# Kernel optimization log

Measured on AMD Instinct MI355X. Metric: run time of the kernel, lower is better.

## Reference

```python
import jax, jax.numpy as jnp
import numpy as np

RES = 64
C_DIM = 64
N_BLOCKS = 4
EPS = 1e-12


def conv2d(x, w, b, pad):
    out = jax.lax.conv_general_dilated(
        x, w, window_strides=(1, 1), padding=[(pad, pad), (pad, pad)],
        dimension_numbers=('NCHW', 'OIHW', 'NCHW'))
    return out + b[None, :, None, None]


def unfold3(x):
    # F.unfold(kernel=3, padding=1): [B,C,H,W] -> [B, C*9, H*W], torch ordering (c, ki, kj)
    B, C, H, W = x.shape
    xp = jnp.pad(x, ((0, 0), (0, 0), (1, 1), (1, 1)))
    patches = jnp.stack([xp[:, :, ki:ki + H, kj:kj + W]
                         for ki in range(3) for kj in range(3)], axis=2)  # [B,C,9,H,W]
    return patches.reshape(B, C * 9, H * W)


def fold3(t, H, W):
    # F.fold(kernel=3, padding=1): sum overlapping patches back to [B,C,H,W]
    B, C9, L = t.shape
    C = C9 // 9
    t = t.reshape(B, C, 3, 3, H, W)
    out = jnp.zeros((B, C, H + 2, W + 2), t.dtype)
    for ki in range(3):
        for kj in range(3):
            out = out.at[:, :, ki:ki + H, kj:kj + W].add(t[:, :, ki, kj])
    return out[:, :, 1:H + 1, 1:W + 1]


def setup_inputs() -> dict:
    key = jax.random.key(0)
    ks = jax.random.split(key, 16)
    B, L, C = 4, RES * RES, C_DIM
    s = 0.05
    inp = {
        'c0': jax.random.normal(ks[0], (B, L, C), jnp.float32),
        'f0': jax.random.normal(ks[1], (B, L, C), jnp.float32),
        'c1': jax.random.normal(ks[2], (B, L, C), jnp.float32),
        'head_w': jax.random.normal(ks[3], (C, C, 5, 5), jnp.float32) * s,
        'head_b': jax.random.normal(ks[4], (C,), jnp.float32) * s,
        'rb_w1': jax.random.normal(ks[5], (N_BLOCKS, C, C, 3, 3), jnp.float32) * s,
        'rb_b1': jax.random.normal(ks[6], (N_BLOCKS, C), jnp.float32) * s,
        'rb_w2': jax.random.normal(ks[7], (N_BLOCKS, C, C, 3, 3), jnp.float32) * s,
        'rb_b2': jax.random.normal(ks[8], (N_BLOCKS, C), jnp.float32) * s,
        'tail_w': jax.random.normal(ks[9], (C, C, 5, 5), jnp.float32) * s,
        'tail_b': jax.random.normal(ks[10], (C,), jnp.float32) * s,
        'sq_w': jax.random.normal(ks[11], (C, 2 * C, 5, 5), jnp.float32) * s,
        'sq_b': jax.random.normal(ks[12], (C,), jnp.float32) * s,
    }
    return inp


def reference(c0, f0, c1, head_w, head_b, rb_w1, rb_b1, rb_w2, rb_b2,
              tail_w, tail_b, sq_w, sq_b):
    B, L, C = c1.shape
    H = W = RES
    c1 = c1.swapaxes(1, 2).reshape(B, C, H, W)
    c0 = c0.swapaxes(1, 2).reshape(B, C, H, W)
    f0 = f0.swapaxes(1, 2).reshape(B, C, H, W)
    Delta_c = c1 - c0

    # --- search_Trans: patch correlation + best-match texture transfer ---
    c1u = unfold3(c1)                       # [B, C9, L]
    c0u = unfold3(c0).swapaxes(1, 2)        # [B, L, C9]
    c0n = c0u / jnp.maximum(jnp.linalg.norm(c0u, axis=2, keepdims=True), EPS)
    c1n = c1u / jnp.maximum(jnp.linalg.norm(c1u, axis=1, keepdims=True), EPS)
    R = jnp.einsum('blk,bkm->blm', c0n, c1n)  # [B, L, L]
    R_star = jnp.max(R, axis=1)               # [B, L]
    R_arg = jnp.argmax(R, axis=1)              # [B, L]
    f0u = unfold3(f0)                          # [B, C9, L]
    Tu = jnp.take_along_axis(f0u, R_arg[:, None, :], axis=2)
    T = fold3(Tu, H, W) / 9.0                  # [B, C, H, W]
    S = R_star.reshape(B, 1, H, W)

    # --- residual conv stack on Delta_c ---
    x1 = conv2d(Delta_c, head_w, head_b, 2)
    x = x1
    for i in range(rb_w1.shape[0]):  # NOTE: original feeds x1 into every block
        h = jax.nn.relu(conv2d(x1, rb_w1[i], rb_b1[i], 1))
        x = conv2d(h, rb_w2[i], rb_b2[i], 1) + x1
    x = conv2d(x, tail_w, tail_b, 2)
    Delta_c_fea = x + x1

    x = conv2d(jnp.concatenate([Delta_c_fea, T], axis=1), sq_w, sq_b, 2)
    out = Delta_c_fea + x * S
    return out.reshape(B, C, L).swapaxes(1, 2)
```

## Files before the change

### kernel.cpp

```cpp
#include <hip/hip_runtime.h>
#include <hip/hip_bf16.h>


#define BATCH 4

typedef unsigned short u16;
typedef unsigned int   u32;
typedef __attribute__((ext_vector_type(8))) short short8;
typedef __attribute__((ext_vector_type(4))) float f32x4;

__device__ __forceinline__ void bsplit2(float a, float b, u32& ho, u32& lo) {
  __hip_bfloat16 ha = __float2bfloat16(a), hb = __float2bfloat16(b);
  float ra = a - __bfloat162float(ha), rb = b - __bfloat162float(hb);
  __hip_bfloat16 la = __float2bfloat16(ra), lb = __float2bfloat16(rb);
  ho = (u32)*(u16*)&ha | ((u32)*(u16*)&hb << 16);
  lo = (u32)*(u16*)&la | ((u32)*(u16*)&lb << 16);
}

__device__ __forceinline__ void gload_lds16(const void* g, void* l) {
  __builtin_amdgcn_global_load_lds((const __attribute__((address_space(1))) void*)g,
                                   (__attribute__((address_space(3))) void*)l, 16, 0, 0);
}

__global__ __launch_bounds__(256) void prep_ss(const float* __restrict__ c0,
    const float* __restrict__ c1, float* __restrict__ ss0, float* __restrict__ ss1)
{
  int tid = blockIdx.x * 256 + threadIdx.x;
  const float* p0 = c0 + (size_t)tid * 64;
  const float* p1 = c1 + (size_t)tid * 64;
  float s0 = 0.f, s1 = 0.f;
  for (int c = 0; c < 64; ++c) {
    float a = p0[c]; s0 += a * a;
    float b = p1[c]; s1 += b * b;
  }
  ss0[tid] = s0;
  ss1[tid] = s1;
}

__global__ __launch_bounds__(256) void norm_kernel(const float* __restrict__ ss0,
    const float* __restrict__ ss1, float* __restrict__ inv0, float* __restrict__ inv1)
{
  int tid = blockIdx.x * 256 + threadIdx.x;
  int b = tid >> 12, l = tid & 4095;
  int y = l >> 6, x = l & 63;
  int base = b << 12;
  float s0 = 0.f, s1 = 0.f;
  for (int dy = -1; dy <= 1; ++dy) {
    int yy = y + dy; if (yy < 0 || yy >= 64) continue;
    for (int dx = -1; dx <= 1; ++dx) {
      int xx = x + dx; if (xx < 0 || xx >= 64) continue;
      int ii = base + (yy << 6) + xx;
      s0 += ss0[ii]; s1 += ss1[ii];
    }
  }
  inv0[tid] = 1.f / fmaxf(sqrtf(s0), 1e-12f);
  inv1[tid] = 1.f / fmaxf(sqrtf(s1), 1e-12f);
}

__global__ __launch_bounds__(256) void split_pad_kernel(const float* __restrict__ c0,
    const float* __restrict__ c1, u16* __restrict__ p0h, u16* __restrict__ p0l,
    u16* __restrict__ p1h, u16* __restrict__ p1l)
{
  int b = blockIdx.y, t = threadIdx.x;
  int pix = blockIdx.x * 4 + (t >> 6);
  int c = t & 63;
  int py = pix / 66, px = pix - py * 66;
  size_t d = ((size_t)b * 4356 + pix) * 64 + c;
  float v0 = 0.f, v1 = 0.f;
  if (py >= 1 && py <= 64 && px >= 1 && px <= 64) {
    size_t s = (((size_t)b << 12) + ((py - 1) << 6) + (px - 1)) * 64 + c;
    v0 = c0[s]; v1 = c1[s];
  }
  __hip_bfloat16 h = __float2bfloat16(v0);
  float r = v0 - __bfloat162float(h);
  __hip_bfloat16 lo = __float2bfloat16(r);
  p0h[d] = *(u16*)&h; p0l[d] = *(u16*)&lo;
  h = __float2bfloat16(v1);
  r = v1 - __bfloat162float(h);
  lo = __float2bfloat16(r);
  p1h[d] = *(u16*)&h; p1l[d] = *(u16*)&lo;
}

__global__ __launch_bounds__(256) void wprep(const float* __restrict__ src,
    u16* __restrict__ wh, u16* __restrict__ wl, int Cin, int KK, int n)
{
  int i = blockIdx.x * 256 + threadIdx.x;
  if (i >= n) return;
  int per = Cin * KK;
  int cout = i / per;
  int rem = i - cout * per;
  int cin = rem / KK;
  int tap = rem - cin * KK;
  float x = src[i];
  __hip_bfloat16 h = __float2bfloat16(x);
  float r = x - __bfloat162float(h);
  __hip_bfloat16 lo = __float2bfloat16(r);
  int d = (tap * 64 + cout) * Cin + cin;
  wh[d] = *(u16*)&h;
  wl[d] = *(u16*)&lo;
}

__global__ __launch_bounds__(256) void corr_mfma(const u16* __restrict__ p0h,
    const u16* __restrict__ p0l, const u16* __restrict__ p1h, const u16* __restrict__ p1l,
    const float* __restrict__ inv0, float* __restrict__ pval, int* __restrict__ pidx)
{
  __shared__ __align__(16) u16 smem[32768];
  int mt = blockIdx.x, lt = blockIdx.y, b = blockIdx.z;
  int t = threadIdx.x;
  int lane = t & 63, w = t >> 6;
  int wl = w >> 1, wm = w & 1;
  int cc = lane & 15, q = lane >> 4;
  const size_t boff = (size_t)b * 278784;
  const u16* msrc = (w == 0) ? p0h : (w == 1) ? p0l : (w == 2) ? p1h : p1l;
  msrc += boff;
  const float* inv0b = inv0 + (b << 12);
  int isB = w >> 1;

  int srow0 = lane >> 2;
  int cs_g  = (lane & 3) ^ ((lane >> 3) & 3);
  int sw    = (cc >> 1) & 3;

  auto stage = [&](int ssub, int sph, u16* dst) {
    int r = sph >> 1, hh = sph & 1;
    int ki = r / 3, kj = r - ki * 3;
    int pb = isB ? (mt << 7) : ((lt << 9) + (ssub << 7));
#pragma unroll
    for (int it = 0; it < 8; ++it) {
      int p = pb + (it << 4) + srow0;
      int ypad = (p >> 6) + ki, xpad = (p & 63) + kj;
      const u16* g = msrc + (((size_t)(ypad * 66 + xpad)) << 6) + (hh << 5) + (cs_g << 3);
      gload_lds16(g, dst + (it << 9));
    }
  };

  float bval[4] = {-1e30f, -1e30f, -1e30f, -1e30f};
  int   bidx[4] = {0, 0, 0, 0};

  stage(0, 0, smem + (w << 12));

  for (int sub = 0; sub < 4; ++sub) {
    int row0 = (lt << 9) + (sub << 7);
    f32x4 acc[4][4];
#pragma unroll
    for (int i = 0; i < 4; ++i)
#pragma unroll
      for (int j = 0; j < 4; ++j) acc[i][j] = (f32x4){0.f, 0.f, 0.f, 0.f};

    for (int ph = 0; ph < 18; ++ph) {
      int g = sub * 18 + ph;
      int nxt = g + 1;
      if (nxt < 72) {
        int np = ph + 1, ns = sub;
        if (np == 18) { np = 0; ++ns; }
        stage(ns, np, smem + ((nxt & 1) << 14) + (w << 12));
        asm volatile("s_waitcnt vmcnt(8)" ::: "memory");
      } else {
        asm volatile("s_waitcnt vmcnt(0)" ::: "memory");
      }
      __builtin_amdgcn_s_barrier();
      __builtin_amdgcn_sched_barrier(0);
      const u16* bb = smem + ((g & 1) << 14);
      short8 afh[4], afl[4], bfh[4], bfl[4];
#pragma unroll
      for (int i = 0; i < 4; ++i) {
        int ra = (((wl << 6) + (i << 4) + cc) << 5) + ((q ^ sw) << 3);
        afh[i] = *(const short8*)(&bb[ra]);
        afl[i] = *(const short8*)(&bb[4096 + ra]);
      }
#pragma unroll
      for (int j = 0; j < 4; ++j) {
        int rb = (((wm << 6) + (j << 4) + cc) << 5) + ((q ^ sw) << 3);
        bfh[j] = *(const short8*)(&bb[8192 + rb]);
        bfl[j] = *(const short8*)(&bb[12288 + rb]);
      }
#pragma unroll
      for (int i = 0; i < 4; ++i)
#pragma unroll
        for (int j = 0; j < 4; ++j) {
          acc[i][j] = __builtin_amdgcn_mfma_f32_16x16x32_bf16(afh[i], bfl[j], acc[i][j], 0, 0, 0);
          acc[i][j] = __builtin_amdgcn_mfma_f32_16x16x32_bf16(afl[i], bfh[j], acc[i][j], 0, 0, 0);
          acc[i][j] = __builtin_amdgcn_mfma_f32_16x16x32_bf16(afh[i], bfh[j], acc[i][j], 0, 0, 0);
        }
      __builtin_amdgcn_sched_barrier(0);
      __builtin_amdgcn_s_barrier();
    }
#pragma unroll
    for (int i = 0; i < 4; ++i) {
#pragma unroll
      for (int rg = 0; rg < 4; ++rg) {
        int l = row0 + (wl << 6) + (i << 4) + (q << 2) + rg;
        float sc = inv0b[l];
#pragma unroll
        for (int j = 0; j < 4; ++j) {
          float v = acc[i][j][rg] * sc;
          if (v > bval[j]) { bval[j] = v; bidx[j] = l; }
        }
      }
    }
  }

  __syncthreads();
  float* lval = (float*)smem;
  int*   lidx = (int*)((char*)smem + 4096);
  int slot = (wl << 2) + q;
#pragma unroll
  for (int j = 0; j < 4; ++j) {
    int col = (wm << 6) + (j << 4) + cc;
    lval[col * 8 + slot] = bval[j];
    lidx[col * 8 + slot] = bidx[j];
  }
  __syncthreads();
  if (t < 128) {
    float bv = -1e30f; int bi = 0x7FFFFFFF;
    for (int s = 0; s < 8; ++s) {
      float v = lval[t * 8 + s]; int id = lidx[t * 8 + s];
      if (v > bv || (v == bv && id < bi)) { bv = v; bi = id; }
    }
    size_t o = (size_t)(((b << 3) + lt) << 12) + (mt << 7) + t;
    pval[o] = bv; pidx[o] = bi;
  }
}

__global__ __launch_bounds__(256) void reduce_kernel(const float* __restrict__ pval,
    const int* __restrict__ pidx, const float* __restrict__ inv1,
    float* __restrict__ S, int* __restrict__ arg)
{
  int tid = blockIdx.x * 256 + threadIdx.x;
  int b = tid >> 12, m = tid & 4095;
  float bv = -1e30f; int bi = 0x7FFFFFFF;
  for (int lt = 0; lt < 8; ++lt) {
    size_t o = (size_t)(((b << 3) + lt) << 12) + m;
    float v = pval[o]; int id = pidx[o];
    if (v > bv || (v == bv && id < bi)) { bv = v; bi = id; }
  }
  S[tid] = bv * inv1[tid];
  arg[tid] = ((unsigned)bi < 4096u) ? bi : 0;
}

__global__ __launch_bounds__(256) void tgather_kernel(const float* __restrict__ f0,
    const int* __restrict__ arg, float* __restrict__ T)
{
  __shared__ int a3[192];
  int y = blockIdx.x, b = blockIdx.y, t = threadIdx.x;
  if (t < 192) {
    int r = t >> 6, xx = t & 63;
    int yy = y + r - 1;
    a3[t] = (yy >= 0 && yy < 64) ? arg[(b << 12) + (yy << 6) + xx] : 0;
  }
  __syncthreads();
  int c = t & 63, pg = t >> 6;
  for (int it = 0; it < 16; ++it) {
    int px = pg + (it << 2);
    float sum = 0.f;
#pragma unroll
    for (int ki = 0; ki < 3; ++ki) {
      int yn = y + 1 - ki;
      if (yn < 0 || yn >= 64) continue;
#pragma unroll
      for (int kj = 0; kj < 3; ++kj) {
        int xn = px + 1 - kj;
        if (xn < 0 || xn >= 64) continue;
        int p = a3[((2 - ki) << 6) + xn];
        int sy = (p >> 6) + ki - 1, sx = (p & 63) + kj - 1;
        if (sy >= 0 && sy < 64 && sx >= 0 && sx < 64)
          sum += f0[((((size_t)b << 12) + (sy << 6) + sx) << 6) + c];
      }
    }
    T[((((size_t)b << 12) + (y << 6) + px)) * 64 + c] = sum * (1.f / 9.f);
  }
}

template<int KS, int CINCH>
__global__ __launch_bounds__(256) void conv_mfma(const float* __restrict__ in0,
    const float* __restrict__ in1, const u16* __restrict__ whp, const u16* __restrict__ wlp,
    const float* __restrict__ bias, float* __restrict__ outp,
    const float* __restrict__ res, int dorelu, int dm)
{
  constexpr int P = KS / 2;
  constexpr int CIN = CINCH * 32;
  constexpr int KSH = (CINCH == 2) ? 1 : 2;
  constexpr int NIT = KS * KS * CINCH;
  __shared__ __align__(16) u16 Ah[2][32 * 40], Al[2][32 * 40];
  __shared__ __align__(16) u16 Bh[2][64 * 40], Bl[2][64 * 40];
  int tile = blockIdx.x, b = blockIdx.y;
  int t = threadIdx.x;
  int lane = t & 63, w = t >> 6;
  int wpx = w >> 1, wm = w & 1;
  int cc = lane & 15, q = lane >> 4;
  int ty = tile >> 1, txb = (tile & 1) << 5;
  const size_t abase = (size_t)b << 12;
  f32x4 acc[2];
  acc[0] = (f32x4){0.f, 0.f, 0.f, 0.f};
  acc[1] = (f32x4){0.f, 0.f, 0.f, 0.f};

  uint4 rg[4];
  int arow = t >> 2, acs = t & 3;
  int tb = t - 128;

  auto issue_loads = [&](int itn) {
    int tapn = itn >> KSH, kkn = itn & (CINCH - 1);
    int ki = tapn / KS, kj = tapn - ki * KS;
    if (t < 128) {
      rg[0] = rg[1] = rg[2] = rg[3] = make_uint4(0u, 0u, 0u, 0u);
      int iy = ty + ki - P;
      int ix = txb + arow + kj - P;
      if ((unsigned)iy < 64u && (unsigned)ix < 64u) {
        size_t base = (abase + (iy << 6) + ix) << 6;
        int cg = kkn * 32 + (acs << 3);
        if (dm) {
          rg[0] = *(const uint4*)(in0 + base + cg);
          rg[1] = *(const uint4*)(in0 + base + cg + 4);
          rg[2] = *(const uint4*)(in1 + base + cg);
          rg[3] = *(const uint4*)(in1 + base + cg + 4);
        } else {
          const float* sp = (CINCH == 4 && cg >= 64) ? (in1 + base + (cg - 64))
                                                     : (in0 + base + cg);
          rg[0] = *(const uint4*)sp;
          rg[1] = *(const uint4*)(sp + 4);
        }
      }
    } else {
#pragma unroll
      for (int rr = 0; rr < 2; ++rr) {
        int idx = tb * 2 + rr;
        int cout = idx >> 2, cs = idx & 3;
        size_t so = (size_t)(tapn * 64 + cout) * CIN + kkn * 32 + (cs << 3);
        rg[rr]     = *(const uint4*)&whp[so];
        rg[2 + rr] = *(const uint4*)&wlp[so];
      }
    }
  };

  auto write_lds = [&](int cur) {
    if (t < 128) {
      float v[8];
      if (dm) {
#pragma unroll
        for (int e = 0; e < 4; ++e) {
          v[e]     = __uint_as_float((&rg[2].x)[e]) - __uint_as_float((&rg[0].x)[e]);
          v[4 + e] = __uint_as_float((&rg[3].x)[e]) - __uint_as_float((&rg[1].x)[e]);
        }
      } else {
#pragma unroll
        for (int e = 0; e < 4; ++e) {
          v[e]     = __uint_as_float((&rg[0].x)[e]);
          v[4 + e] = __uint_as_float((&rg[1].x)[e]);
        }
      }
      uint4 uh, ul;
      bsplit2(v[0], v[1], uh.x, ul.x);
      bsplit2(v[2], v[3], uh.y, ul.y);
      bsplit2(v[4], v[5], uh.z, ul.z);
      bsplit2(v[6], v[7], uh.w, ul.w);
      *(uint4*)&Ah[cur][arow * 40 + (acs << 3)] = uh;
      *(uint4*)&Al[cur][arow * 40 + (acs << 3)] = ul;
    } else {
#pragma unroll
      for (int rr = 0; rr < 2; ++rr) {
        int idx = tb * 2 + rr;
        int cout = idx >> 2, cs = idx & 3;
        *(uint4*)&Bh[cur][cout * 40 + (cs << 3)] = rg[rr];
        *(uint4*)&Bl[cur][cout * 40 + (cs << 3)] = rg[2 + rr];
      }
    }
  };

  issue_loads(0);
  for (int it = 0; it < NIT; ++it) {
    int cur = it & 1;
    write_lds(cur);
    if (it + 1 < NIT) issue_loads(it + 1);
    asm volatile("s_waitcnt lgkmcnt(0)" ::: "memory");
    __builtin_amdgcn_s_barrier();
    __builtin_amdgcn_sched_barrier(0);
    short8 afh, afl, bfh[2], bfl[2];
    {
      int ra = ((wpx << 4) + cc) * 40 + (q << 3);
      afh = *(const short8*)&Ah[cur][ra];
      afl = *(const short8*)&Al[cur][ra];
    }
#pragma unroll
    for (int j = 0; j < 2; ++j) {
      int rb = ((wm << 5) + (j << 4) + cc) * 40 + (q << 3);
      bfh[j] = *(const short8*)&Bh[cur][rb];
      bfl[j] = *(const short8*)&Bl[cur][rb];
    }
#pragma unroll
    for (int j = 0; j < 2; ++j) {
      acc[j] = __builtin_amdgcn_mfma_f32_16x16x32_bf16(afh, bfl[j], acc[j], 0, 0, 0);
      acc[j] = __builtin_amdgcn_mfma_f32_16x16x32_bf16(afl, bfh[j], acc[j], 0, 0, 0);
      acc[j] = __builtin_amdgcn_mfma_f32_16x16x32_bf16(afh, bfh[j], acc[j], 0, 0, 0);
    }
  }
#pragma unroll
  for (int rgi = 0; rgi < 4; ++rgi) {
    int p = (ty << 6) + txb + (wpx << 4) + (q << 2) + rgi;
#pragma unroll
    for (int j = 0; j < 2; ++j) {
      int cout = (wm << 5) + (j << 4) + cc;
      float v = acc[j][rgi] + bias[cout];
      if (dorelu) v = fmaxf(v, 0.f);
      size_t oi = ((abase + p) << 6) + cout;
      if (res) v += res[oi];
      outp[oi] = v;
    }
  }
}

__global__ __launch_bounds__(256) void final_kernel(const float* __restrict__ dcf,
    const float* __restrict__ xs, const float* __restrict__ S, float* __restrict__ out)
{
  int tid = blockIdx.x * 256 + threadIdx.x;
  out[tid] = dcf[tid] + xs[tid] * S[tid >> 6];
}

extern "C" void kernel_launch(void* const* d_in, const int* in_sizes, int n_in,
                              void* d_out, int out_size, void* d_ws, size_t ws_size,
                              hipStream_t stream)
{
  (void)in_sizes; (void)n_in; (void)out_size; (void)ws_size;
  const float* c0     = (const float*)d_in[0];
  const float* f0     = (const float*)d_in[1];
  const float* c1     = (const float*)d_in[2];
  const float* head_w = (const float*)d_in[3];
  const float* head_b = (const float*)d_in[4];
  const float* rb_w1  = (const float*)d_in[5];
  const float* rb_b1  = (const float*)d_in[6];
  const float* rb_w2  = (const float*)d_in[7];
  const float* rb_b2  = (const float*)d_in[8];
  const float* tail_w = (const float*)d_in[9];
  const float* tail_b = (const float*)d_in[10];
  const float* sq_w   = (const float*)d_in[11];
  const float* sq_b   = (const float*)d_in[12];
  float* out = (float*)d_out;
  char* ws = (char*)d_ws;

  const size_t OFF_SS0  = 0;
  const size_t OFF_SS1  = 65536;
  const size_t OFF_INV0 = 131072;
  const size_t OFF_INV1 = 196608;
  const size_t OFF_S    = 262144;
  const size_t OFF_ARG  = 327680;
  const size_t OFF_PVAL = 393216;
  const size_t OFF_PIDX = 917504;
  const size_t OFF_WHH  = 1441792;
  const size_t OFF_WHL  = 1646592;
  const size_t OFF_W1H  = 1851392;
  const size_t OFF_W1L  = 1925120;
  const size_t OFF_W2H  = 1998848;
  const size_t OFF_W2L  = 2072576;
  const size_t OFF_WTH  = 2146304;
  const size_t OFF_WTL  = 2351104;
  const size_t OFF_WSH  = 2555904;
  const size_t OFF_WSL  = 2965504;
  const size_t OFF_P0H  = 3375104;
  const size_t OFF_P0L  = OFF_P0H + 2230272;
  const size_t OFF_P1H  = OFF_P0L + 2230272;
  const size_t OFF_P1L  = OFF_P1H + 2230272;
  const size_t OFF_SA   = 3375104;
  const size_t OFF_SB   = 7569408;
  const size_t OFF_SC   = 11763712;

  float* ss0  = (float*)(ws + OFF_SS0);
  float* ss1  = (float*)(ws + OFF_SS1);
  float* inv0 = (float*)(ws + OFF_INV0);
  float* inv1 = (float*)(ws + OFF_INV1);
  float* Sbuf = (float*)(ws + OFF_S);
  int*   argb = (int*)(ws + OFF_ARG);
  float* pval = (float*)(ws + OFF_PVAL);
  int*   pidx = (int*)(ws + OFF_PIDX);
  u16* whh = (u16*)(ws + OFF_WHH); u16* whl = (u16*)(ws + OFF_WHL);
  u16* w1h = (u16*)(ws + OFF_W1H); u16* w1l = (u16*)(ws + OFF_W1L);
  u16* w2h = (u16*)(ws + OFF_W2H); u16* w2l = (u16*)(ws + OFF_W2L);
  u16* wth = (u16*)(ws + OFF_WTH); u16* wtl = (u16*)(ws + OFF_WTL);
  u16* wsh = (u16*)(ws + OFF_WSH); u16* wsl = (u16*)(ws + OFF_WSL);
  u16* p0h = (u16*)(ws + OFF_P0H); u16* p0l = (u16*)(ws + OFF_P0L);
  u16* p1h = (u16*)(ws + OFF_P1H); u16* p1l = (u16*)(ws + OFF_P1L);
  float* x1  = (float*)(ws + OFF_SA);
  float* Tb  = (float*)(ws + OFF_SA);
  float* hb  = (float*)(ws + OFF_SB);
  float* dcf = (float*)(ws + OFF_SB);
  float* xb  = (float*)(ws + OFF_SC);
  float* xsb = (float*)(ws + OFF_SC);

  dim3 b256(256);
  prep_ss<<<dim3(64), b256, 0, stream>>>(c0, c1, ss0, ss1);
  norm_kernel<<<dim3(64), b256, 0, stream>>>(ss0, ss1, inv0, inv1);
  split_pad_kernel<<<dim3(1089, BATCH), b256, 0, stream>>>(c0, c1, p0h, p0l, p1h, p1l);
  wprep<<<dim3(400), b256, 0, stream>>>(head_w, whh, whl, 64, 25, 102400);
  wprep<<<dim3(144), b256, 0, stream>>>(rb_w1 + 110592, w1h, w1l, 64, 9, 36864);
  wprep<<<dim3(144), b256, 0, stream>>>(rb_w2 + 110592, w2h, w2l, 64, 9, 36864);
  wprep<<<dim3(400), b256, 0, stream>>>(tail_w, wth, wtl, 64, 25, 102400);
  wprep<<<dim3(800), b256, 0, stream>>>(sq_w, wsh, wsl, 128, 25, 204800);

  corr_mfma<<<dim3(32, 8, BATCH), b256, 0, stream>>>(p0h, p0l, p1h, p1l, inv0, pval, pidx);
  reduce_kernel<<<dim3(64), b256, 0, stream>>>(pval, pidx, inv1, Sbuf, argb);

  dim3 cgrid(128, BATCH);
  conv_mfma<5, 2><<<cgrid, b256, 0, stream>>>(c0, c1, whh, whl, head_b, x1, nullptr, 0, 1);
  conv_mfma<3, 2><<<cgrid, b256, 0, stream>>>(x1, nullptr, w1h, w1l, rb_b1 + 192, hb, nullptr, 1, 0);
  conv_mfma<3, 2><<<cgrid, b256, 0, stream>>>(hb, nullptr, w2h, w2l, rb_b2 + 192, xb, x1, 0, 0);
  conv_mfma<5, 2><<<cgrid, b256, 0, stream>>>(xb, nullptr, wth, wtl, tail_b, dcf, x1, 0, 0);

  tgather_kernel<<<dim3(64, BATCH), b256, 0, stream>>>(f0, argb, Tb);
  conv_mfma<5, 4><<<cgrid, b256, 0, stream>>>(dcf, Tb, wsh, wsl, sq_b, xsb, nullptr, 0, 0);

  final_kernel<<<dim3(4096), b256, 0, stream>>>(dcf, xsb, Sbuf, out);
}
```

Baseline: 529.4 us.

## Fuse sum-of-squares into split_pad, widen conv K-step, fuse final epilogue

The per-pixel sum-of-squares is now computed inside split_pad_kernel with a wave shuffle reduction, which removes the separate prep_ss pass over c0/c1. The conv_mfma main loop now consumes 64 input channels per iteration instead of 32, with an LDS stride of 72. This halves the number of barriers and loop iterations at the cost of more registers. The final out = dcf + x*S step moves into the squeeze conv's epilogue, removing final_kernel and one intermediate buffer round trip. Register pressure from rg[8] and v[16] may reduce occupancy.

```diff
diff --git a/kernel.cpp b/kernel.cpp
--- a/kernel.cpp
+++ b/kernel.cpp
@@ -20,21 +20,6 @@
 __device__ __forceinline__ void gload_lds16(const void* g, void* l) {
   __builtin_amdgcn_global_load_lds((const __attribute__((address_space(1))) void*)g,
                                    (__attribute__((address_space(3))) void*)l, 16, 0, 0);
-}
-
-__global__ __launch_bounds__(256) void prep_ss(const float* __restrict__ c0,
-    const float* __restrict__ c1, float* __restrict__ ss0, float* __restrict__ ss1)
-{
-  int tid = blockIdx.x * 256 + threadIdx.x;
-  const float* p0 = c0 + (size_t)tid * 64;
-  const float* p1 = c1 + (size_t)tid * 64;
-  float s0 = 0.f, s1 = 0.f;
-  for (int c = 0; c < 64; ++c) {
-    float a = p0[c]; s0 += a * a;
-    float b = p1[c]; s1 += b * b;
-  }
-  ss0[tid] = s0;
-  ss1[tid] = s1;
 }
 
 __global__ __launch_bounds__(256) void norm_kernel(const float* __restrict__ ss0,
@@ -59,15 +44,17 @@
 
 __global__ __launch_bounds__(256) void split_pad_kernel(const float* __restrict__ c0,
     const float* __restrict__ c1, u16* __restrict__ p0h, u16* __restrict__ p0l,
-    u16* __restrict__ p1h, u16* __restrict__ p1l)
+    u16* __restrict__ p1h, u16* __restrict__ p1l,
+    float* __restrict__ ss0, float* __restrict__ ss1)
 {
   int b = blockIdx.y, t = threadIdx.x;
   int pix = blockIdx.x * 4 + (t >> 6);
   int c = t & 63;
   int py = pix / 66, px = pix - py * 66;
   size_t d = ((size_t)b * 4356 + pix) * 64 + c;
+  bool interior = (py >= 1 && py <= 64 && px >= 1 && px <= 64);
   float v0 = 0.f, v1 = 0.f;
-  if (py >= 1 && py <= 64 && px >= 1 && px <= 64) {
+  if (interior) {
     size_t s = (((size_t)b << 12) + ((py - 1) << 6) + (px - 1)) * 64 + c;
     v0 = c0[s]; v1 = c1[s];
   }
@@ -79,6 +66,17 @@
   r = v1 - __bfloat162float(h);
   lo = __float2bfloat16(r);
   p1h[d] = *(u16*)&h; p1l[d] = *(u16*)&lo;
+  float s0 = v0 * v0, s1 = v1 * v1;
+#pragma unroll
+  for (int off = 32; off; off >>= 1) {
+    s0 += __shfl_xor(s0, off);
+    s1 += __shfl_xor(s1, off);
+  }
+  if (c == 0 && interior) {
+    int sstid = (b << 12) + ((py - 1) << 6) + (px - 1);
+    ss0[sstid] = s0;
+    ss1[sstid] = s1;
+  }
 }
 
 __global__ __launch_bounds__(256) void wprep(const float* __restrict__ src,
@@ -274,14 +272,15 @@
 __global__ __launch_bounds__(256) void conv_mfma(const float* __restrict__ in0,
     const float* __restrict__ in1, const u16* __restrict__ whp, const u16* __restrict__ wlp,
     const float* __restrict__ bias, float* __restrict__ outp,
-    const float* __restrict__ res, int dorelu, int dm)
+    const float* __restrict__ res, const float* __restrict__ smul, int dorelu, int dm)
 {
   constexpr int P = KS / 2;
   constexpr int CIN = CINCH * 32;
-  constexpr int KSH = (CINCH == 2) ? 1 : 2;
-  constexpr int NIT = KS * KS * CINCH;
-  __shared__ __align__(16) u16 Ah[2][32 * 40], Al[2][32 * 40];
-  __shared__ __align__(16) u16 Bh[2][64 * 40], Bl[2][64 * 40];
+  constexpr int NKH = CINCH / 2;
+  constexpr int NIT = KS * KS * NKH;
+  constexpr int AST = 72;
+  __shared__ __align__(16) u16 Ah[2][32 * AST], Al[2][32 * AST];
+  __shared__ __align__(16) u16 Bh[2][64 * AST], Bl[2][64 * AST];
   int tile = blockIdx.x, b = blockIdx.y;
   int t = threadIdx.x;
   int lane = t & 63, w = t >> 6;
@@ -293,74 +292,82 @@
   acc[0] = (f32x4){0.f, 0.f, 0.f, 0.f};
   acc[1] = (f32x4){0.f, 0.f, 0.f, 0.f};
 
-  uint4 rg[4];
+  uint4 rg[8];
   int arow = t >> 2, acs = t & 3;
   int tb = t - 128;
+  int brow = tb >> 1, bhalf = tb & 1;
 
   auto issue_loads = [&](int itn) {
-    int tapn = itn >> KSH, kkn = itn & (CINCH - 1);
+    int tapn = (NKH == 1) ? itn : (itn >> 1);
+    int kh   = (NKH == 1) ? 0 : (itn & 1);
     int ki = tapn / KS, kj = tapn - ki * KS;
     if (t < 128) {
-      rg[0] = rg[1] = rg[2] = rg[3] = make_uint4(0u, 0u, 0u, 0u);
+#pragma unroll
+      for (int k = 0; k < 8; ++k) rg[k] = make_uint4(0u, 0u, 0u, 0u);
       int iy = ty + ki - P;
       int ix = txb + arow + kj - P;
       if ((unsigned)iy < 64u && (unsigned)ix < 64u) {
         size_t base = (abase + (iy << 6) + ix) << 6;
-        int cg = kkn * 32 + (acs << 3);
+        int cg = kh * 64 + acs * 16;
         if (dm) {
-          rg[0] = *(const uint4*)(in0 + base + cg);
-          rg[1] = *(const uint4*)(in0 + base + cg + 4);
-          rg[2] = *(const uint4*)(in1 + base + cg);
-          rg[3] = *(const uint4*)(in1 + base + cg + 4);
+#pragma unroll
+          for (int k = 0; k < 4; ++k) {
+            rg[k]     = *(const uint4*)(in0 + base + cg + 4 * k);
+            rg[4 + k] = *(const uint4*)(in1 + base + cg + 4 * k);
+          }
         } else {
-          const float* sp = (CINCH == 4 && cg >= 64) ? (in1 + base + (cg - 64))
-                                                     : (in0 + base + cg);
-          rg[0] = *(const uint4*)sp;
-          rg[1] = *(const uint4*)(sp + 4);
+          const float* sp = (CINCH == 4 && kh == 1) ? (in1 + base + (cg - 64))
+                                                    : (in0 + base + cg);
+#pragma unroll
+          for (int k = 0; k < 4; ++k) rg[k] = *(const uint4*)(sp + 4 * k);
         }
       }
     } else {
-#pragma unroll
-      for (int rr = 0; rr < 2; ++rr) {
-        int idx = tb * 2 + rr;
-        int cout = idx >> 2, cs = idx & 3;
-        size_t so = (size_t)(tapn * 64 + cout) * CIN + kkn * 32 + (cs << 3);
-        rg[rr]     = *(const uint4*)&whp[so];
-        rg[2 + rr] = *(const uint4*)&wlp[so];
+      size_t so = (size_t)(tapn * 64 + brow) * CIN + kh * 64 + bhalf * 32;
+#pragma unroll
+      for (int k = 0; k < 4; ++k) {
+        rg[k]     = *(const uint4*)&whp[so + 8 * k];
+        rg[4 + k] = *(const uint4*)&wlp[so + 8 * k];
       }
     }
   };
 
   auto write_lds = [&](int cur) {
     if (t < 128) {
-      float v[8];
+      float v[16];
       if (dm) {
 #pragma unroll
-        for (int e = 0; e < 4; ++e) {
-          v[e]     = __uint_as_float((&rg[2].x)[e]) - __uint_as_float((&rg[0].x)[e]);
-          v[4 + e] = __uint_as_float((&rg[3].x)[e]) - __uint_as_float((&rg[1].x)[e]);
-        }
+        for (int k = 0; k < 4; ++k)
+#pragma unroll
+          for (int e = 0; e < 4; ++e)
+            v[k * 4 + e] = __uint_as_float((&rg[4 + k].x)[e]) - __uint_as_float((&rg[k].x)[e]);
       } else {
 #pragma unroll
-        for (int e = 0; e < 4; ++e) {
-          v[e]     = __uint_as_float((&rg[0].x)[e]);
-          v[4 + e] = __uint_as_float((&rg[1].x)[e]);
-        }
-      }
-      uint4 uh, ul;
-      bsplit2(v[0], v[1], uh.x, ul.x);
-      bsplit2(v[2], v[3], uh.y, ul.y);
-      bsplit2(v[4], v[5], uh.z, ul.z);
-      bsplit2(v[6], v[7], uh.w, ul.w);
-      *(uint4*)&Ah[cur][arow * 40 + (acs << 3)] = uh;
-      *(uint4*)&Al[cur][arow * 40 + (acs << 3)] = ul;
+        for (int k = 0; k < 4; ++k)
+#pragma unroll
+          for (int e = 0; e < 4; ++e)
+            v[k * 4 + e] = __uint_as_float((&rg[k].x)[e]);
+      }
+      uint4 uh0, ul0, uh1, ul1;
+      bsplit2(v[0], v[1], uh0.x, ul0.x);
+      bsplit2(v[2], v[3], uh0.y, ul0.y);
+      bsplit2(v[4], v[5], uh0.z, ul0.z);
+      bsplit2(v[6], v[7], uh0.w, ul0.w);
+      bsplit2(v[8], v[9], uh1.x, ul1.x);
+      bsplit2(v[10], v[11], uh1.y, ul1.y);
+      bsplit2(v[12], v[13], uh1.z, ul1.z);
+      bsplit2(v[14], v[15], uh1.w, ul1.w);
+      int o = arow * AST + acs * 16;
+      *(uint4*)&Ah[cur][o]     = uh0;
+      *(uint4*)&Ah[cur][o + 8] = uh1;
+      *(uint4*)&Al[cur][o]     = ul0;
+      *(uint4*)&Al[cur][o + 8] = ul1;
     } else {
-#pragma unroll
-      for (int rr = 0; rr < 2; ++rr) {
-        int idx = tb * 2 + rr;
-        int cout = idx >> 2, cs = idx & 3;
-        *(uint4*)&Bh[cur][cout * 40 + (cs << 3)] = rg[rr];
-        *(uint4*)&Bl[cur][cout * 40 + (cs << 3)] = rg[2 + rr];
+      int o = brow * AST + bhalf * 32;
+#pragma unroll
+      for (int k = 0; k < 4; ++k) {
+        *(uint4*)&Bh[cur][o + 8 * k] = rg[k];
+        *(uint4*)&Bl[cur][o + 8 * k] = rg[4 + k];
       }
     }
   };
@@ -373,23 +380,27 @@
     asm volatile("s_waitcnt lgkmcnt(0)" ::: "memory");
     __builtin_amdgcn_s_barrier();
     __builtin_amdgcn_sched_barrier(0);
-    short8 afh, afl, bfh[2], bfl[2];
-    {
-      int ra = ((wpx << 4) + cc) * 40 + (q << 3);
-      afh = *(const short8*)&Ah[cur][ra];
-      afl = *(const short8*)&Al[cur][ra];
-    }
-#pragma unroll
-    for (int j = 0; j < 2; ++j) {
-      int rb = ((wm << 5) + (j << 4) + cc) * 40 + (q << 3);
-      bfh[j] = *(const short8*)&Bh[cur][rb];
-      bfl[j] = *(const short8*)&Bl[cur][rb];
-    }
-#pragma unroll
-    for (int j = 0; j < 2; ++j) {
-      acc[j] = __builtin_amdgcn_mfma_f32_16x16x32_bf16(afh, bfl[j], acc[j], 0, 0, 0);
-      acc[j] = __builtin_amdgcn_mfma_f32_16x16x32_bf16(afl, bfh[j], acc[j], 0, 0, 0);
-      acc[j] = __builtin_amdgcn_mfma_f32_16x16x32_bf16(afh, bfh[j], acc[j], 0, 0, 0);
+    short8 afh[2], afl[2], bfh[2][2], bfl[2][2];
+#pragma unroll
+    for (int ks = 0; ks < 2; ++ks) {
+      int ra = ((wpx << 4) + cc) * AST + ks * 32 + (q << 3);
+      afh[ks] = *(const short8*)&Ah[cur][ra];
+      afl[ks] = *(const short8*)&Al[cur][ra];
+#pragma unroll
+      for (int j = 0; j < 2; ++j) {
+        int rb = ((wm << 5) + (j << 4) + cc) * AST + ks * 32 + (q << 3);
+        bfh[j][ks] = *(const short8*)&Bh[cur][rb];
+        bfl[j][ks] = *(const short8*)&Bl[cur][rb];
+      }
+    }
+#pragma unroll
+    for (int ks = 0; ks < 2; ++ks) {
+      acc[0] = __builtin_amdgcn_mfma_f32_16x16x32_bf16(afh[ks], bfl[0][ks], acc[0], 0, 0, 0);
+      acc[1] = __builtin_amdgcn_mfma_f32_16x16x32_bf16(afh[ks], bfl[1][ks], acc[1], 0, 0, 0);
+      acc[0] = __builtin_amdgcn_mfma_f32_16x16x32_bf16(afl[ks], bfh[0][ks], acc[0], 0, 0, 0);
+      acc[1] = __builtin_amdgcn_mfma_f32_16x16x32_bf16(afl[ks], bfh[1][ks], acc[1], 0, 0, 0);
+      acc[0] = __builtin_amdgcn_mfma_f32_16x16x32_bf16(afh[ks], bfh[0][ks], acc[0], 0, 0, 0);
+      acc[1] = __builtin_amdgcn_mfma_f32_16x16x32_bf16(afh[ks], bfh[1][ks], acc[1], 0, 0, 0);
     }
   }
 #pragma unroll
@@ -401,17 +412,11 @@
       float v = acc[j][rgi] + bias[cout];
       if (dorelu) v = fmaxf(v, 0.f);
       size_t oi = ((abase + p) << 6) + cout;
-      if (res) v += res[oi];
+      if (smul) v = res[oi] + v * smul[abase + p];
+      else if (res) v += res[oi];
       outp[oi] = v;
     }
   }
-}
-
-__global__ __launch_bounds__(256) void final_kernel(const float* __restrict__ dcf,
-    const float* __restrict__ xs, const float* __restrict__ S, float* __restrict__ out)
-{
-  int tid = blockIdx.x * 256 + threadIdx.x;
-  out[tid] = dcf[tid] + xs[tid] * S[tid >> 6];
 }
 
 extern "C" void kernel_launch(void* const* d_in, const int* in_sizes, int n_in,
@@ -481,12 +486,10 @@
   float* hb  = (float*)(ws + OFF_SB);
   float* dcf = (float*)(ws + OFF_SB);
   float* xb  = (float*)(ws + OFF_SC);
-  float* xsb = (float*)(ws + OFF_SC);
 
   dim3 b256(256);
-  prep_ss<<<dim3(64), b256, 0, stream>>>(c0, c1, ss0, ss1);
+  split_pad_kernel<<<dim3(1089, BATCH), b256, 0, stream>>>(c0, c1, p0h, p0l, p1h, p1l, ss0, ss1);
   norm_kernel<<<dim3(64), b256, 0, stream>>>(ss0, ss1, inv0, inv1);
-  split_pad_kernel<<<dim3(1089, BATCH), b256, 0, stream>>>(c0, c1, p0h, p0l, p1h, p1l);
   wprep<<<dim3(400), b256, 0, stream>>>(head_w, whh, whl, 64, 25, 102400);
   wprep<<<dim3(144), b256, 0, stream>>>(rb_w1 + 110592, w1h, w1l, 64, 9, 36864);
   wprep<<<dim3(144), b256, 0, stream>>>(rb_w2 + 110592, w2h, w2l, 64, 9, 36864);
@@ -497,13 +500,11 @@
   reduce_kernel<<<dim3(64), b256, 0, stream>>>(pval, pidx, inv1, Sbuf, argb);
 
   dim3 cgrid(128, BATCH);
-  conv_mfma<5, 2><<<cgrid, b256, 0, stream>>>(c0, c1, whh, whl, head_b, x1, nullptr, 0, 1);
-  conv_mfma<3, 2><<<cgrid, b256, 0, stream>>>(x1, nullptr, w1h, w1l, rb_b1 + 192, hb, nullptr, 1, 0);
-  conv_mfma<3, 2><<<cgrid, b256, 0, stream>>>(hb, nullptr, w2h, w2l, rb_b2 + 192, xb, x1, 0, 0);
-  conv_mfma<5, 2><<<cgrid, b256, 0, stream>>>(xb, nullptr, wth, wtl, tail_b, dcf, x1, 0, 0);
+  conv_mfma<5, 2><<<cgrid, b256, 0, stream>>>(c0, c1, whh, whl, head_b, x1, nullptr, nullptr, 0, 1);
+  conv_mfma<3, 2><<<cgrid, b256, 0, stream>>>(x1, nullptr, w1h, w1l, rb_b1 + 192, hb, nullptr, nullptr, 1, 0);
+  conv_mfma<3, 2><<<cgrid, b256, 0, stream>>>(hb, nullptr, w2h, w2l, rb_b2 + 192, xb, x1, nullptr, 0, 0);
+  conv_mfma<5, 2><<<cgrid, b256, 0, stream>>>(xb, nullptr, wth, wtl, tail_b, dcf, x1, nullptr, 0, 0);
 
   tgather_kernel<<<dim3(64, BATCH), b256, 0, stream>>>(f0, argb, Tb);
-  conv_mfma<5, 4><<<cgrid, b256, 0, stream>>>(dcf, Tb, wsh, wsl, sq_b, xsb, nullptr, 0, 0);
-
-  final_kernel<<<dim3(4096), b256, 0, stream>>>(dcf, xsb, Sbuf, out);
-}
+  conv_mfma<5, 4><<<cgrid, b256, 0, stream>>>(dcf, Tb, wsh, wsl, sq_b, out, dcf, Sbuf, 0, 0);
+}
```

After: 514.4 us. 2.8% less time.
